# Kernel tuning notes

Measured on AMD Instinct MI355X. Metric: run time of the kernel, lower is better.

## Reference

```python
import jax, jax.numpy as jnp
import numpy as np

D_MODEL = 1024
N_HEADS = 16
D_K = D_MODEL // N_HEADS


def _xavier(key, shape):
    fan_in, fan_out = shape[1], shape[0]
    a = np.sqrt(6.0 / (fan_in + fan_out))
    return jax.random.uniform(key, shape, jnp.float32, -a, a)


def setup_inputs() -> dict:
    key = jax.random.key(0)
    kx, kq, kk, kv, ko = jax.random.split(key, 5)
    x = jax.random.normal(kx, (2, 2048, D_MODEL), jnp.float32)
    # nn.Linear weights are [out, in]; y = x @ W.T
    Wq = _xavier(kq, (D_MODEL, D_MODEL))
    Wk = _xavier(kk, (D_MODEL, D_MODEL))
    Wv = _xavier(kv, (D_MODEL, D_MODEL))
    Wo = _xavier(ko, (D_MODEL, D_MODEL))
    bo = jnp.zeros((D_MODEL,), jnp.float32)
    return {"x": x, "Wq": Wq, "Wk": Wk, "Wv": Wv, "Wo": Wo, "bo": bo}


def reference(x, Wq, Wk, Wv, Wo, bo):
    B, S, D = x.shape
    def split_heads(t):
        # [B,S,D] -> [B,H,S,d_k]
        return t.reshape(B, S, N_HEADS, D_K).transpose(0, 2, 1, 3)
    Q = split_heads(x @ Wq.T)
    K = split_heads(x @ Wk.T)
    V = split_heads(x @ Wv.T)
    scale = 1.0 / jnp.sqrt(jnp.asarray(D_K, x.dtype))
    scores = jnp.einsum('bhqd,bhkd->bhqk', Q, K) * scale  # [B,H,S,S]
    attn = jax.nn.softmax(scores, axis=-1)
    out = jnp.einsum('bhqk,bhkd->bhqd', attn, V)  # [B,H,S,d_k]
    out = out.transpose(0, 2, 1, 3).reshape(B, S, D)  # merge heads
    return out @ Wo.T + bo
```

## Files before the change

### kernel.cpp

```cpp
#include <hip/hip_runtime.h>


typedef __attribute__((ext_vector_type(8))) short bf16x8;
typedef __attribute__((ext_vector_type(4))) short bf16x4;
typedef __attribute__((ext_vector_type(4))) float f32x4;
typedef __attribute__((ext_vector_type(2))) unsigned int u32x2;

#define GK 1024
#define SEQ 2048
#define NHEAD 16
#define DKD 64
#define PADW 72

#define MFMA32(a, b, c) __builtin_amdgcn_mfma_f32_16x16x32_bf16((a), (b), (c), 0, 0, 0)

#if __has_builtin(__builtin_amdgcn_mfma_f32_16x16x16bf16_1k)
#define HAVE_MFMA16 1
#define MFMA16(a, b, c) __builtin_amdgcn_mfma_f32_16x16x16bf16_1k((a), (b), (c), 0, 0, 0)
#else
#define HAVE_MFMA16 0
#endif

#if __has_builtin(__builtin_amdgcn_exp2f)
#define EXP2(x) __builtin_amdgcn_exp2f(x)
#else
#define EXP2(x) exp2f(x)
#endif

#define QSCALE 0.18033688011f

static __device__ __forceinline__ unsigned short f2bf(float f) {
    unsigned int u = __float_as_uint(f);
    u += 0x7fffu + ((u >> 16) & 1u);
    return (unsigned short)(u >> 16);
}

static __device__ __forceinline__ unsigned int pack_bf2(float a, float b) {
    unsigned int ua = __float_as_uint(a) + 0x8000u;
    unsigned int ub = __float_as_uint(b) + 0x8000u;
    return __builtin_amdgcn_perm(ub, ua, 0x07060302u);
}

__global__ __launch_bounds__(256) void cast_all(const float* __restrict__ x,
                                                const float* __restrict__ wq,
                                                const float* __restrict__ wk,
                                                const float* __restrict__ wv,
                                                const float* __restrict__ wo,
                                                unsigned short* __restrict__ Xb,
                                                unsigned short* __restrict__ Wqkv,
                                                unsigned short* __restrict__ Wob) {
    const int bid = blockIdx.x;
    const float* src; unsigned short* dst; int off;
    if (bid < 4096)      { src = x;  dst = Xb;             off = bid; }
    else if (bid < 5120) { src = wq; dst = Wqkv;           off = bid - 4096; }
    else if (bid < 6144) { src = wk; dst = Wqkv + 1048576; off = bid - 5120; }
    else if (bid < 7168) { src = wv; dst = Wqkv + 2097152; off = bid - 6144; }
    else                 { src = wo; dst = Wob;            off = bid - 7168; }
    const int i = off * 1024 + threadIdx.x * 4;
    float4 v = *(const float4*)(src + i);
    u32x2 p; p.x = pack_bf2(v.x, v.y); p.y = pack_bf2(v.z, v.w);
    *(u32x2*)(dst + i) = p;
}

template <int MODE>
__global__ __launch_bounds__(256) void gemm_bt(const unsigned short* __restrict__ A,
                                               const unsigned short* __restrict__ Bw,
                                               unsigned short* __restrict__ outb,
                                               float* __restrict__ outf,
                                               const float* __restrict__ bias) {
    __shared__ __align__(16) unsigned short As[128 * 32];
    __shared__ __align__(16) unsigned short Bs[128 * 32];
    __shared__ __align__(16) unsigned short E[(MODE == 0) ? 4 * 64 * PADW : 4];

    const int t    = threadIdx.x;
    const int lane = t & 63;
    const int w    = t >> 6;
    const int wm   = (w >> 1) * 64;
    const int wn   = (w & 1) * 64;
    const int bm0  = blockIdx.x * 128;
    const int bn0  = blockIdx.y * 128;
    const int lm   = lane & 15;
    const int lq   = lane >> 4;
    const int kc   = lq * 8;

    const unsigned short* Ab = A + (size_t)bm0 * GK;
    const unsigned short* Bb = Bw + (size_t)bn0 * GK;

    f32x4 acc[4][4];
#pragma unroll
    for (int i = 0; i < 4; i++)
#pragma unroll
        for (int j = 0; j < 4; j++) acc[i][j] = (f32x4){0.f, 0.f, 0.f, 0.f};

    const int q_uni = (t & ~63);

    for (int k0 = 0; k0 < GK; k0 += 32) {
        __syncthreads();
#pragma unroll
        for (int i = 0; i < 2; ++i) {
            int q = i * 256 + t;
            int r = q >> 2;
            int c = (q & 3) * 8;
            int q0 = i * 256 + q_uni;
            __builtin_amdgcn_global_load_lds(
                (const __attribute__((address_space(1))) void*)(Ab + (size_t)r * GK + k0 + c),
                (__attribute__((address_space(3))) void*)(As + (size_t)q0 * 8),
                16, 0, 0);
            __builtin_amdgcn_global_load_lds(
                (const __attribute__((address_space(1))) void*)(Bb + (size_t)r * GK + k0 + c),
                (__attribute__((address_space(3))) void*)(Bs + (size_t)q0 * 8),
                16, 0, 0);
        }
        __syncthreads();

        bf16x8 af[4], bf[4];
#pragma unroll
        for (int i = 0; i < 4; i++)
            af[i] = *(const bf16x8*)(As + (wm + i * 16 + lm) * 32 + kc);
#pragma unroll
        for (int j = 0; j < 4; j++)
            bf[j] = *(const bf16x8*)(Bs + (wn + j * 16 + lm) * 32 + kc);
#pragma unroll
        for (int i = 0; i < 4; i++)
#pragma unroll
            for (int j = 0; j < 4; j++)
                acc[i][j] = MFMA32(af[i], bf[j], acc[i][j]);
    }

    if (MODE == 0) {
        unsigned short* Ew = E + w * (64 * PADW);
        const int nbase = bn0 + wn;
        const int which = nbase >> 10;
        const int hh    = (nbase & 1023) >> 6;
        if (which != 2) {
            const float sc = (which == 0) ? QSCALE : 1.0f;
#pragma unroll
            for (int i = 0; i < 4; i++)
#pragma unroll
                for (int j = 0; j < 4; j++)
#pragma unroll
                    for (int r = 0; r < 4; r++)
                        Ew[(i * 16 + lq * 4 + r) * PADW + j * 16 + lm] =
                            f2bf(acc[i][j][r] * sc);
            unsigned short* dst = outb + (size_t)which * 4194304;
#pragma unroll
            for (int rep = 0; rep < 8; ++rep) {
                const int mm = rep * 8 + (lane >> 3);
                const int d0 = (lane & 7) * 8;
                uint4 v = *(const uint4*)(Ew + mm * PADW + d0);
                const int m_g = bm0 + wm + mm;
                const int b = m_g >> 11, s = m_g & 2047;
                *(uint4*)(dst + (((size_t)(b * NHEAD + hh)) * SEQ + s) * DKD + d0) = v;
            }
        } else {
#pragma unroll
            for (int i = 0; i < 4; i++)
#pragma unroll
                for (int j = 0; j < 4; j++) {
                    u32x2 pk;
                    pk.x = pack_bf2(acc[i][j][0], acc[i][j][1]);
                    pk.y = pack_bf2(acc[i][j][2], acc[i][j][3]);
                    *(u32x2*)(Ew + (j * 16 + lm) * PADW + i * 16 + lq * 4) = pk;
                }
            unsigned short* dst = outb + (size_t)2 * 4194304;
#pragma unroll
            for (int rep = 0; rep < 8; ++rep) {
                const int nn = rep * 8 + (lane >> 3);
                const int mc = (lane & 7) * 8;
                uint4 v = *(const uint4*)(Ew + nn * PADW + mc);
                const int m_g = bm0 + wm + mc;
                const int b = m_g >> 11, s0 = m_g & 2047;
                *(uint4*)(dst + (((size_t)(b * NHEAD + hh)) * DKD + nn) * SEQ + s0) = v;
            }
        }
    } else {
#pragma unroll
        for (int i = 0; i < 4; i++) {
            const int mbase = bm0 + wm + i * 16 + lq * 4;
#pragma unroll
            for (int j = 0; j < 4; j++) {
                const int n = bn0 + wn + j * 16 + lm;
#pragma unroll
                for (int r = 0; r < 4; r++)
                    outf[(size_t)(mbase + r) * 1024 + n] = acc[i][j][r] + bias[n];
            }
        }
    }
}

__global__ __launch_bounds__(256) void attn_kernel(const unsigned short* __restrict__ Qg,
                                                   const unsigned short* __restrict__ Kg,
                                                   const unsigned short* __restrict__ Vtg,
                                                   unsigned short* __restrict__ Og) {
    __shared__ __align__(16) unsigned short KV[2][2][64 * PADW];
#if !HAVE_MFMA16
    __shared__ __align__(16) unsigned short Ps[128 * PADW];
#endif

    const int blk = blockIdx.x;
    const int qb  = blk & 15;
    const int bh  = blk >> 4;
    const unsigned short* Qp  = Qg  + ((size_t)bh * SEQ + qb * 128) * DKD;
    const unsigned short* Kp  = Kg  + (size_t)bh * SEQ * DKD;
    const unsigned short* Vtp = Vtg + (size_t)bh * DKD * SEQ;

    const int t    = threadIdx.x;
    const int lane = t & 63;
    const int w    = t >> 6;
    const int lm   = lane & 15;
    const int kq   = lane >> 4;
    const int qw   = w * 32;

    bf16x8 aq[2][2];
#pragma unroll
    for (int iq = 0; iq < 2; ++iq)
#pragma unroll
        for (int kk = 0; kk < 2; ++kk)
            aq[iq][kk] = *(const bf16x8*)(Qp + (size_t)(qw + iq * 16 + lm) * DKD + kk * 32 + kq * 8);

    f32x4 o[2][4];
    f32x4 ls[2];
#pragma unroll
    for (int iq = 0; iq < 2; ++iq) {
        ls[iq] = (f32x4){0.f, 0.f, 0.f, 0.f};
#pragma unroll
        for (int dj = 0; dj < 4; ++dj) o[iq][dj] = (f32x4){0.f, 0.f, 0.f, 0.f};
    }

    const int sr = t >> 2, sc = (t & 3) * 16;
    uint4 kreg0, kreg1, vreg0, vreg1;
    {
        const unsigned short* kp = Kp + (size_t)sr * DKD + sc;
        const unsigned short* vp = Vtp + (size_t)sr * SEQ + sc;
        uint4 a0 = *(const uint4*)(kp),     a1 = *(const uint4*)(kp + 8);
        uint4 b0 = *(const uint4*)(vp),     b1 = *(const uint4*)(vp + 8);
        uint4* dk = (uint4*)(&KV[0][0][sr * PADW + sc]); dk[0] = a0; dk[1] = a1;
        uint4* dv = (uint4*)(&KV[0][1][sr * PADW + sc]); dv[0] = b0; dv[1] = b1;
    }
    {
        const unsigned short* kp = Kp + (size_t)(64 + sr) * DKD + sc;
        kreg0 = *(const uint4*)(kp); kreg1 = *(const uint4*)(kp + 8);
        const unsigned short* vp = Vtp + (size_t)sr * SEQ + 64 + sc;
        vreg0 = *(const uint4*)(vp); vreg1 = *(const uint4*)(vp + 8);
    }

    for (int kt = 0; kt < 32; ++kt) {
        __syncthreads();
        if (kt + 1 < 32) {
            uint4* dk = (uint4*)(&KV[(kt + 1) & 1][0][sr * PADW + sc]);
            dk[0] = kreg0; dk[1] = kreg1;
            uint4* dv = (uint4*)(&KV[(kt + 1) & 1][1][sr * PADW + sc]);
            dv[0] = vreg0; dv[1] = vreg1;
        }
        if (kt + 2 < 32) {
            const unsigned short* kp = Kp + (size_t)((kt + 2) * 64 + sr) * DKD + sc;
            kreg0 = *(const uint4*)(kp); kreg1 = *(const uint4*)(kp + 8);
            const unsigned short* vp = Vtp + (size_t)sr * SEQ + (kt + 2) * 64 + sc;
            vreg0 = *(const uint4*)(vp); vreg1 = *(const uint4*)(vp + 8);
        }
        const unsigned short* Kc = &KV[kt & 1][0][0];
        const unsigned short* Vc = &KV[kt & 1][1][0];

        f32x4 s[4][2];
#pragma unroll
        for (int jk = 0; jk < 4; ++jk)
#pragma unroll
            for (int iq = 0; iq < 2; ++iq) s[jk][iq] = (f32x4){0.f, 0.f, 0.f, 0.f};
#pragma unroll
        for (int jk = 0; jk < 4; ++jk) {
            bf16x8 ak0 = *(const bf16x8*)(Kc + (jk * 16 + lm) * PADW + kq * 8);
            bf16x8 ak1 = *(const bf16x8*)(Kc + (jk * 16 + lm) * PADW + 32 + kq * 8);
#pragma unroll
            for (int iq = 0; iq < 2; ++iq) {
                s[jk][iq] = MFMA32(ak0, aq[iq][0], s[jk][iq]);
                s[jk][iq] = MFMA32(ak1, aq[iq][1], s[jk][iq]);
            }
        }

#pragma unroll
        for (int jk = 0; jk < 4; ++jk)
#pragma unroll
            for (int iq = 0; iq < 2; ++iq) {
#pragma unroll
                for (int r = 0; r < 4; ++r) s[jk][iq][r] = EXP2(s[jk][iq][r]);
                ls[iq] += s[jk][iq];
            }

#if HAVE_MFMA16
        bf16x4 ap[4][2];
#pragma unroll
        for (int jk = 0; jk < 4; ++jk)
#pragma unroll
            for (int iq = 0; iq < 2; ++iq) {
                u32x2 pk;
                pk.x = pack_bf2(s[jk][iq][0], s[jk][iq][1]);
                pk.y = pack_bf2(s[jk][iq][2], s[jk][iq][3]);
                ap[jk][iq] = __builtin_bit_cast(bf16x4, pk);
            }
#pragma unroll
        for (int dj = 0; dj < 4; ++dj)
#pragma unroll
            for (int jk = 0; jk < 4; ++jk) {
                bf16x4 bv = *(const bf16x4*)(Vc + (dj * 16 + lm) * PADW + jk * 16 + kq * 4);
#pragma unroll
                for (int iq = 0; iq < 2; ++iq)
                    o[iq][dj] = MFMA16(ap[jk][iq], bv, o[iq][dj]);
            }
#else
#pragma unroll
        for (int iq = 0; iq < 2; ++iq)
#pragma unroll
            for (int jk = 0; jk < 4; ++jk) {
                u32x2 pk;
                pk.x = pack_bf2(s[jk][iq][0], s[jk][iq][1]);
                pk.y = pack_bf2(s[jk][iq][2], s[jk][iq][3]);
                *(u32x2*)(Ps + (qw + iq * 16 + lm) * PADW + jk * 16 + kq * 4) = pk;
            }
        bf16x8 ap[2][2];
#pragma unroll
        for (int iq = 0; iq < 2; ++iq)
#pragma unroll
            for (int kk = 0; kk < 2; ++kk)
                ap[iq][kk] = *(const bf16x8*)(Ps + (qw + iq * 16 + lm) * PADW + kk * 32 + kq * 8);
#pragma unroll
        for (int dj = 0; dj < 4; ++dj) {
            bf16x8 bv0 = *(const bf16x8*)(Vc + (dj * 16 + lm) * PADW + kq * 8);
            bf16x8 bv1 = *(const bf16x8*)(Vc + (dj * 16 + lm) * PADW + 32 + kq * 8);
#pragma unroll
            for (int iq = 0; iq < 2; ++iq) {
                o[iq][dj] = MFMA32(ap[iq][0], bv0, o[iq][dj]);
                o[iq][dj] = MFMA32(ap[iq][1], bv1, o[iq][dj]);
            }
        }
#endif
    }

    const int b = bh >> 4, h = bh & 15;
    float linv[2];
#pragma unroll
    for (int iq = 0; iq < 2; ++iq) {
        float l = (ls[iq][0] + ls[iq][1]) + (ls[iq][2] + ls[iq][3]);
        l += __shfl_xor(l, 16);
        l += __shfl_xor(l, 32);
#if __has_builtin(__builtin_amdgcn_rcpf)
        linv[iq] = __builtin_amdgcn_rcpf(l);
#else
        linv[iq] = 1.0f / l;
#endif
    }
#pragma unroll
    for (int iq = 0; iq < 2; ++iq) {
#pragma unroll
        for (int r = 0; r < 4; ++r) {
            const float lv = __shfl(linv[iq], kq * 4 + r);
            const int qrow = qb * 128 + qw + iq * 16 + kq * 4 + r;
            unsigned short* op = Og + (((size_t)(b * SEQ + qrow)) * NHEAD + h) * DKD;
#pragma unroll
            for (int dj = 0; dj < 4; ++dj)
                op[dj * 16 + lm] = f2bf(o[iq][dj][r] * lv);
        }
    }
}

extern "C" void kernel_launch(void* const* d_in, const int* in_sizes, int n_in,
                              void* d_out, int out_size, void* d_ws, size_t ws_size,
                              hipStream_t stream) {
    const float* x  = (const float*)d_in[0];
    const float* Wq = (const float*)d_in[1];
    const float* Wk = (const float*)d_in[2];
    const float* Wv = (const float*)d_in[3];
    const float* Wo = (const float*)d_in[4];
    const float* bo = (const float*)d_in[5];
    float* out = (float*)d_out;

    unsigned short* ws = (unsigned short*)d_ws;
    unsigned short* Xb   = ws;
    unsigned short* Wqkv = ws + 4194304;
    unsigned short* Wob  = ws + 7340032;
    unsigned short* QKV  = ws + 8388608;
    unsigned short* Ob   = ws + 20971520;

    cast_all<<<8192, 256, 0, stream>>>(x, Wq, Wk, Wv, Wo, Xb, Wqkv, Wob);
    gemm_bt<0><<<dim3(32, 24), 256, 0, stream>>>(Xb, Wqkv, QKV, nullptr, nullptr);
    attn_kernel<<<512, 256, 0, stream>>>(QKV, QKV + 4194304, QKV + 8388608, Ob);
    gemm_bt<1><<<dim3(32, 8), 256, 0, stream>>>(Ob, Wob, nullptr, out, bo);
}
```

Measured before the change: 204.6 us.

## Narrow output GEMM tile, remap attention blocks per XCD, reorder PV loop

The output-projection GEMM now uses 128x64 tiles, which doubles its grid from 256 to 512 blocks so more CUs have work. The attention kernel remaps block indices so that the blocks placed on each XCD share four batch-heads, aiming for better L2 reuse of K/V. The PV MFMA loop order is swapped so the jk dimension is outermost. The narrower tiles give each block less reuse of the A operand.

```diff
diff --git a/kernel.cpp b/kernel.cpp
--- a/kernel.cpp
+++ b/kernel.cpp
@@ -62,23 +62,24 @@
     *(u32x2*)(dst + i) = p;
 }
 
-template <int MODE>
+template <int MODE, int BN>
 __global__ __launch_bounds__(256) void gemm_bt(const unsigned short* __restrict__ A,
                                                const unsigned short* __restrict__ Bw,
                                                unsigned short* __restrict__ outb,
                                                float* __restrict__ outf,
                                                const float* __restrict__ bias) {
+    constexpr int NJ = BN / 32;
     __shared__ __align__(16) unsigned short As[128 * 32];
-    __shared__ __align__(16) unsigned short Bs[128 * 32];
+    __shared__ __align__(16) unsigned short Bs[BN * 32];
     __shared__ __align__(16) unsigned short E[(MODE == 0) ? 4 * 64 * PADW : 4];
 
     const int t    = threadIdx.x;
     const int lane = t & 63;
     const int w    = t >> 6;
     const int wm   = (w >> 1) * 64;
-    const int wn   = (w & 1) * 64;
+    const int wn   = (w & 1) * (BN / 2);
     const int bm0  = blockIdx.x * 128;
-    const int bn0  = blockIdx.y * 128;
+    const int bn0  = blockIdx.y * BN;
     const int lm   = lane & 15;
     const int lq   = lane >> 4;
     const int kc   = lq * 8;
@@ -86,11 +87,11 @@
     const unsigned short* Ab = A + (size_t)bm0 * GK;
     const unsigned short* Bb = Bw + (size_t)bn0 * GK;
 
-    f32x4 acc[4][4];
+    f32x4 acc[4][NJ];
 #pragma unroll
     for (int i = 0; i < 4; i++)
 #pragma unroll
-        for (int j = 0; j < 4; j++) acc[i][j] = (f32x4){0.f, 0.f, 0.f, 0.f};
+        for (int j = 0; j < NJ; j++) acc[i][j] = (f32x4){0.f, 0.f, 0.f, 0.f};
 
     const int q_uni = (t & ~63);
 
@@ -106,6 +107,13 @@
                 (const __attribute__((address_space(1))) void*)(Ab + (size_t)r * GK + k0 + c),
                 (__attribute__((address_space(3))) void*)(As + (size_t)q0 * 8),
                 16, 0, 0);
+        }
+#pragma unroll
+        for (int i = 0; i < BN / 64; ++i) {
+            int q = i * 256 + t;
+            int r = q >> 2;
+            int c = (q & 3) * 8;
+            int q0 = i * 256 + q_uni;
             __builtin_amdgcn_global_load_lds(
                 (const __attribute__((address_space(1))) void*)(Bb + (size_t)r * GK + k0 + c),
                 (__attribute__((address_space(3))) void*)(Bs + (size_t)q0 * 8),
@@ -113,17 +121,17 @@
         }
         __syncthreads();
 
-        bf16x8 af[4], bf[4];
+        bf16x8 af[4], bf[NJ];
 #pragma unroll
         for (int i = 0; i < 4; i++)
             af[i] = *(const bf16x8*)(As + (wm + i * 16 + lm) * 32 + kc);
 #pragma unroll
-        for (int j = 0; j < 4; j++)
+        for (int j = 0; j < NJ; j++)
             bf[j] = *(const bf16x8*)(Bs + (wn + j * 16 + lm) * 32 + kc);
 #pragma unroll
         for (int i = 0; i < 4; i++)
 #pragma unroll
-            for (int j = 0; j < 4; j++)
+            for (int j = 0; j < NJ; j++)
                 acc[i][j] = MFMA32(af[i], bf[j], acc[i][j]);
     }
 
@@ -178,7 +186,7 @@
         for (int i = 0; i < 4; i++) {
             const int mbase = bm0 + wm + i * 16 + lq * 4;
 #pragma unroll
-            for (int j = 0; j < 4; j++) {
+            for (int j = 0; j < NJ; j++) {
                 const int n = bn0 + wn + j * 16 + lm;
 #pragma unroll
                 for (int r = 0; r < 4; r++)
@@ -197,9 +205,11 @@
     __shared__ __align__(16) unsigned short Ps[128 * PADW];
 #endif
 
-    const int blk = blockIdx.x;
-    const int qb  = blk & 15;
-    const int bh  = blk >> 4;
+    const int id  = blockIdx.x;
+    const int xcd = id & 7;
+    const int j8  = id >> 3;
+    const int bh  = xcd * 4 + (j8 & 3);
+    const int qb  = j8 >> 2;
     const unsigned short* Qp  = Qg  + ((size_t)bh * SEQ + qb * 128) * DKD;
     const unsigned short* Kp  = Kg  + (size_t)bh * SEQ * DKD;
     const unsigned short* Vtp = Vtg + (size_t)bh * DKD * SEQ;
@@ -232,8 +242,8 @@
     {
         const unsigned short* kp = Kp + (size_t)sr * DKD + sc;
         const unsigned short* vp = Vtp + (size_t)sr * SEQ + sc;
-        uint4 a0 = *(const uint4*)(kp),     a1 = *(const uint4*)(kp + 8);
-        uint4 b0 = *(const uint4*)(vp),     b1 = *(const uint4*)(vp + 8);
+        uint4 a0 = *(const uint4*)(kp), a1 = *(const uint4*)(kp + 8);
+        uint4 b0 = *(const uint4*)(vp), b1 = *(const uint4*)(vp + 8);
         uint4* dk = (uint4*)(&KV[0][0][sr * PADW + sc]); dk[0] = a0; dk[1] = a1;
         uint4* dv = (uint4*)(&KV[0][1][sr * PADW + sc]); dv[0] = b0; dv[1] = b1;
     }
@@ -298,9 +308,9 @@
                 ap[jk][iq] = __builtin_bit_cast(bf16x4, pk);
             }
 #pragma unroll
-        for (int dj = 0; dj < 4; ++dj)
-#pragma unroll
-            for (int jk = 0; jk < 4; ++jk) {
+        for (int jk = 0; jk < 4; ++jk)
+#pragma unroll
+            for (int dj = 0; dj < 4; ++dj) {
                 bf16x4 bv = *(const bf16x4*)(Vc + (dj * 16 + lm) * PADW + jk * 16 + kq * 4);
 #pragma unroll
                 for (int iq = 0; iq < 2; ++iq)
@@ -381,7 +391,7 @@
     unsigned short* Ob   = ws + 20971520;
 
     cast_all<<<8192, 256, 0, stream>>>(x, Wq, Wk, Wv, Wo, Xb, Wqkv, Wob);
-    gemm_bt<0><<<dim3(32, 24), 256, 0, stream>>>(Xb, Wqkv, QKV, nullptr, nullptr);
+    gemm_bt<0, 128><<<dim3(32, 24), 256, 0, stream>>>(Xb, Wqkv, QKV, nullptr, nullptr);
     attn_kernel<<<512, 256, 0, stream>>>(QKV, QKV + 4194304, QKV + 8388608, Ob);
-    gemm_bt<1><<<dim3(32, 8), 256, 0, stream>>>(Ob, Wob, nullptr, out, bo);
-}
+    gemm_bt<1, 64><<<dim3(32, 16), 256, 0, stream>>>(Ob, Wob, nullptr, out, bo);
+}
```

After: 199.2 us. 1.03x faster.
